# Optimization experiments

Measured on AMD Instinct MI355X. Metric: run time of the kernel, lower is better.

The kernel has to match this reference:

```python
import jax, jax.numpy as jnp
import numpy as np

N = 100000
E = 1600000
IN, HID, OUT = 128, 32, 32


def gcn_conv(x, ei, ew, W, b, n):
    # PyG GCNConv: symmetric norm with self-loops, edge_attr as edge weight
    h = x @ W                                  # [n, d_out]
    row, col = ei[0], ei[1]
    loop = jnp.arange(n)
    row = jnp.concatenate([row, loop])
    col = jnp.concatenate([col, loop])
    ew = jnp.concatenate([ew, jnp.ones((n,), ew.dtype)])
    deg = jax.ops.segment_sum(ew, col, num_segments=n)
    dinv = jnp.where(deg > 0, jax.lax.rsqrt(deg), 0.0)
    norm = dinv[row] * ew * dinv[col]          # [E+n]
    out = jax.ops.segment_sum(norm[:, None] * h[row], col, num_segments=n)
    return out + b


def setup_inputs() -> dict:
    key = jax.random.key(0)
    ks = jax.random.split(key, 24)
    inp = {}
    for i in range(3):
        inp[f"x{i+1}"] = jax.random.normal(ks[i], (N, IN), jnp.float32)
        inp[f"ei{i+1}"] = jax.random.randint(ks[3 + i], (2, E), 0, N, jnp.int64)
        inp[f"ea{i+1}"] = jax.random.uniform(ks[6 + i], (E,), jnp.float32)
        inp[f"W{i+1}"] = jax.random.normal(ks[9 + i], (IN, HID), jnp.float32) * (IN ** -0.5)
        inp[f"b{i+1}"] = jnp.zeros((HID,), jnp.float32)
        inp[f"Wo{i+1}"] = jax.random.normal(ks[12 + i], (HID, OUT), jnp.float32) * (HID ** -0.5)
        inp[f"bo{i+1}"] = jnp.zeros((OUT,), jnp.float32)
    inp["att_w"] = jax.random.normal(ks[15], (HID, 1), jnp.float32) * (HID ** -0.5)
    return inp


def reference(x1, x2, x3, ei1, ei2, ei3, ea1, ea2, ea3,
              W1, W2, W3, b1, b2, b3,
              Wo1, Wo2, Wo3, bo1, bo2, bo3, att_w):
    xs = [x1, x2, x3]
    eis = [ei1, ei2, ei3]
    eas = [ea1, ea2, ea3]
    Ws = [W1, W2, W3]
    bs = [b1, b2, b3]
    Wos = [Wo1, Wo2, Wo3]
    bos = [bo1, bo2, bo3]

    embs, coefs = [], []
    for x, ei, ea, W, b in zip(xs, eis, eas, Ws, bs):
        e = jax.nn.relu(gcn_conv(x, ei, ea, W, b, N))   # [N, HID]; dropout is eval no-op
        embs.append(e)
        coefs.append(jnp.exp(jax.nn.leaky_relu(e @ att_w)))  # [N, 1]
    coef_sum = coefs[0] + coefs[1] + coefs[2]
    weights = [c / coef_sum for c in coefs]
    h = sum(w * e for w, e in zip(weights, embs))       # [N, HID]

    out = sum(gcn_conv(h, ei, ea, Wo, bo, N)
              for ei, ea, Wo, bo in zip(eis, eas, Wos, bos))
    return (out, weights[0], weights[1], weights[2])
```

## Files before the change

### kernel.cpp

```cpp
#include <hip/hip_runtime.h>
#include <hip/hip_fp16.h>

typedef unsigned short u16;
typedef unsigned int   u32;
typedef _Float16 h2 __attribute__((ext_vector_type(2)));

#define N_NODES 100000
#define N_EDGES 1600000
#define IN_DIM  128
#define HID_DIM 32
#define OUT_DIM 32

#define BK   512
#define NBC  196
#define NBT  (3 * NBC)

#define PB    256
#define BINB  1024
#define CHUNK 18750
#define SC_N  (NBT * PB)
#define SC_CHUNK 2048
#define SC_G  ((SC_N + SC_CHUNK - 1) / SC_CHUNK)
#define GN4  ((N_NODES * 4 + 255) / 256)
#define MM2  ((N_NODES + 63) / 64)

#define KEYB 4
#define NKEY (BK << KEYB)

__device__ inline int ofs_at(const int* __restrict__ rp1, const int* __restrict__ bs, int m) {
    return m ? rp1[m] + bs[(m - 1) >> 11] : 0;
}


__global__ void binhist_kernel(const int* __restrict__ ei0, const int* __restrict__ ei1,
                               const int* __restrict__ ei2, int* __restrict__ hist_t) {
    __shared__ int hloc[NBT];
    for (int i = threadIdx.x; i < NBT; i += blockDim.x) hloc[i] = 0;
    __syncthreads();
    int b = blockIdx.x;
    int beg = b * CHUNK, end = beg + CHUNK;
    for (int e = beg + threadIdx.x; e < end; e += blockDim.x) {
        int c = (e >= 2 * N_EDGES) ? 2 : (e >= N_EDGES ? 1 : 0);
        const int* ei = (c == 0) ? ei0 : (c == 1) ? ei1 : ei2;
        int col = ei[N_EDGES + (e - c * N_EDGES)];
        atomicAdd(&hloc[c * NBC + (col >> 9)], 1);
    }
    __syncthreads();
    for (int g = threadIdx.x; g < NBT; g += blockDim.x)
        hist_t[g * PB + b] = hloc[g];
}


__global__ void scan1_kernel(const int* __restrict__ counts, int* __restrict__ rp1,
                             int* __restrict__ blocksum) {
    __shared__ int wsum[4];
    int tid = threadIdx.x;
    int base = blockIdx.x * SC_CHUNK + tid * 8;
    int vals[8];
    int tsum = 0;
    if (base < SC_N) {
        int4 v0 = *(const int4*)(counts + base);
        int4 v1 = *(const int4*)(counts + base + 4);
        vals[0] = v0.x; vals[1] = v0.y; vals[2] = v0.z; vals[3] = v0.w;
        vals[4] = v1.x; vals[5] = v1.y; vals[6] = v1.z; vals[7] = v1.w;
#pragma unroll
        for (int k = 0; k < 8; k++) tsum += vals[k];
    } else {
#pragma unroll
        for (int k = 0; k < 8; k++) vals[k] = 0;
    }
    int lane = tid & 63, wave = tid >> 6;
    int x = tsum;
    for (int d = 1; d < 64; d <<= 1) {
        int t = __shfl_up(x, d, 64);
        if (lane >= d) x += t;
    }
    if (lane == 63) wsum[wave] = x;
    __syncthreads();
    int woff = 0;
    for (int w = 0; w < wave; w++) woff += wsum[w];
    int run = woff + x - tsum;
    if (base < SC_N) {
#pragma unroll
        for (int k = 0; k < 8; k++) {
            run += vals[k];
            rp1[base + k + 1] = run;
        }
    }
    if (tid == blockDim.x - 1) blocksum[blockIdx.x] = woff + x;
    if (blockIdx.x == 0 && tid == 0) rp1[0] = 0;
}

__global__ void scan2_kernel(int* __restrict__ blocksum, int n) {
    __shared__ int wsum[4];
    int tid = threadIdx.x;
    int lane = tid & 63, wave = tid >> 6;
    int carry = 0;
    for (int base = 0; base < n; base += 256) {
        int i = base + tid;
        int v = (i < n) ? blocksum[i] : 0;
        int x = v;
        for (int d = 1; d < 64; d <<= 1) {
            int t = __shfl_up(x, d, 64);
            if (lane >= d) x += t;
        }
        if (lane == 63) wsum[wave] = x;
        __syncthreads();
        int woff = 0;
        for (int w = 0; w < wave; w++) woff += wsum[w];
        int total = wsum[0] + wsum[1] + wsum[2] + wsum[3];
        if (i < n) blocksum[i] = carry + woff + x - v;
        carry += total;
        __syncthreads();
    }
}


__global__ void binscatter_kernel(const int* __restrict__ ei0, const int* __restrict__ ei1,
                                  const int* __restrict__ ei2,
                                  const float* __restrict__ ea0, const float* __restrict__ ea1,
                                  const float* __restrict__ ea2,
                                  const int* __restrict__ rp1, const int* __restrict__ bsum,
                                  int2* __restrict__ stg) {
    __shared__ int base_l[NBT];
    int b = blockIdx.x;
    for (int g = threadIdx.x; g < NBT; g += blockDim.x)
        base_l[g] = ofs_at(rp1, bsum, g * PB + b);
    __syncthreads();
    int beg = b * CHUNK, end = beg + CHUNK;
    for (int e = beg + threadIdx.x; e < end; e += blockDim.x) {
        int c = (e >= 2 * N_EDGES) ? 2 : (e >= N_EDGES ? 1 : 0);
        int le = e - c * N_EDGES;
        const int* ei = (c == 0) ? ei0 : (c == 1) ? ei1 : ei2;
        const float* ea = (c == 0) ? ea0 : (c == 1) ? ea1 : ea2;
        int row = ei[le];
        int col = ei[N_EDGES + le];
        int g = c * NBC + (col >> 9);
        int slot = atomicAdd(&base_l[g], 1);
        stg[slot] = make_int2(row | ((col & 511) << 17), __float_as_int(ea[le]));
    }
}


__global__ void bucket_sort_kernel(const int2* __restrict__ stg, const int* __restrict__ rp1,
                                   const int* __restrict__ bsum,
                                   u32* __restrict__ csr,
                                   float* __restrict__ dinv, int* __restrict__ row_ptr) {
    __shared__ int hist[NKEY];
    __shared__ int colStart[BK];
    __shared__ float deg[BK];
    __shared__ float dl[BK];
    __shared__ int wsum[4];
    int tid = threadIdx.x;
    int g = blockIdx.x;
    int c = g / NBC;
    int colBase = (g % NBC) << 9;
    for (int i = tid; i < NKEY; i += 256) hist[i] = 0;
    deg[tid] = 1.0f;
    deg[tid + 256] = 1.0f;
    __syncthreads();
    int beg = ofs_at(rp1, bsum, g * PB);
    int end = (g == NBT - 1) ? 3 * N_EDGES : ofs_at(rp1, bsum, (g + 1) * PB);
    int cnt = end - beg;
    for (int i = tid; i < cnt; i += blockDim.x) {
        int2 p = stg[beg + i];
        int cl = (p.x >> 17) & 511;
        int row = p.x & 0x1FFFF;
        atomicAdd(&hist[(cl << KEYB) | (row >> 13)], 1);
        atomicAdd(&deg[cl], __int_as_float(p.y));
    }
    __syncthreads();
    int base32 = tid * 32;
    int v[32]; int tsum = 0;
#pragma unroll
    for (int k = 0; k < 32; k++) { v[k] = hist[base32 + k]; tsum += v[k]; }
    int lane = tid & 63, wave = tid >> 6;
    int xs = tsum;
    for (int d = 1; d < 64; d <<= 1) {
        int tt = __shfl_up(xs, d, 64);
        if (lane >= d) xs += tt;
    }
    if (lane == 63) wsum[wave] = xs;
    __syncthreads();
    int woff = 0;
    for (int w = 0; w < wave; w++) woff += wsum[w];
    int run = woff + xs - tsum;
#pragma unroll
    for (int k = 0; k < 32; k++) {
        if (k == 0)  colStart[2 * tid]     = run;
        if (k == 16) colStart[2 * tid + 1] = run;
        int t2 = v[k]; hist[base32 + k] = run; run += t2;
    }
    dl[tid] = rsqrtf(deg[tid]);
    dl[tid + 256] = rsqrtf(deg[tid + 256]);
    __syncthreads();
    for (int i = tid; i < cnt; i += blockDim.x) {
        int2 p = stg[beg + i];
        int cl = (p.x >> 17) & 511;
        int row = p.x & 0x1FFFF;
        int key = (cl << KEYB) | (row >> 13);
        int slot = atomicAdd(&hist[key], 1);
        float vv = __int_as_float(p.y) * dl[cl];
        __half h = __float2half(vv);
        u32 hb = (u32)(*(u16*)&h) & 0x7FFF;
        csr[beg + slot] = (u32)row | (hb << 17);
    }
#pragma unroll
    for (int q = 0; q < 2; q++) {
        int cl = tid + q * 256;
        int col = colBase + cl;
        if (col < N_NODES) {
            dinv[(size_t)c * N_NODES + col] = dl[cl];
            row_ptr[(size_t)c * N_NODES + col] = beg + colStart[cl];
        }
    }
    if (g == NBT - 1 && tid == 0) row_ptr[3 * N_NODES] = 3 * N_EDGES;
}


__device__ inline u32 pack_half2(float a, float b) {
    __half2 h = __floats2half2_rn(a, b);
    union { __half2 h; u32 u; } cv; cv.h = h;
    return cv.u;
}

__device__ inline float2 unpack_half2(u32 u) {
    union { u32 u; __half2 h; } cv; cv.u = u;
    return __half22float2(cv.h);
}

__device__ inline float val15(u32 meta) {
    return unpack_half2(meta >> 17).x;
}

__device__ inline float fdot2h(u32 a, u32 b, float c) {
    union { u32 u; h2 h; } ca, cb; ca.u = a; cb.u = b;
    return __builtin_amdgcn_fdot2(ca.h, cb.h, c, false);
}


__global__ void matmul_in3_kernel(const float* __restrict__ x0, const float* __restrict__ x1,
                                  const float* __restrict__ x2,
                                  const float* __restrict__ W0, const float* __restrict__ W1,
                                  const float* __restrict__ W2,
                                  const float* __restrict__ dinv,
                                  u16* __restrict__ h3) {
    __shared__ u32 Ws2[(IN_DIM / 2) * HID_DIM];
    int c = blockIdx.x / MM2;
    int lb = blockIdx.x % MM2;
    const float* x = (c == 0) ? x0 : (c == 1) ? x1 : x2;
    const float* W = (c == 0) ? W0 : (c == 1) ? W1 : W2;
    for (int i = threadIdx.x; i < (IN_DIM / 2) * HID_DIM; i += blockDim.x) {
        int d = i & 31, jp = i >> 5;
        Ws2[i] = pack_half2(W[(2 * jp) * HID_DIM + d], W[(2 * jp + 1) * HID_DIM + d]);
    }
    __syncthreads();
    int t = threadIdx.x & 7;
    int grp = threadIdx.x >> 3;
    int v0 = lb * 64 + grp * 2;
    if (v0 >= N_NODES) return;
    float a[2][4];
#pragma unroll
    for (int k = 0; k < 2; k++)
#pragma unroll
        for (int d = 0; d < 4; d++) a[k][d] = 0.f;
    const float* xr0 = x + (size_t)v0 * IN_DIM;
    const float* xr1 = xr0 + IN_DIM;
#pragma unroll 4
    for (int q = 0; q < 32; q++) {
        float4 xv0 = *(const float4*)(xr0 + 4 * q);
        float4 xv1 = *(const float4*)(xr1 + 4 * q);
        u32 p00 = pack_half2(xv0.x, xv0.y), p01 = pack_half2(xv0.z, xv0.w);
        u32 p10 = pack_half2(xv1.x, xv1.y), p11 = pack_half2(xv1.z, xv1.w);
        uint4 wA = *(const uint4*)&Ws2[(2 * q) * HID_DIM + 4 * t];
        uint4 wB = *(const uint4*)&Ws2[(2 * q + 1) * HID_DIM + 4 * t];
        a[0][0] = fdot2h(p00, wA.x, a[0][0]); a[0][1] = fdot2h(p00, wA.y, a[0][1]);
        a[0][2] = fdot2h(p00, wA.z, a[0][2]); a[0][3] = fdot2h(p00, wA.w, a[0][3]);
        a[0][0] = fdot2h(p01, wB.x, a[0][0]); a[0][1] = fdot2h(p01, wB.y, a[0][1]);
        a[0][2] = fdot2h(p01, wB.z, a[0][2]); a[0][3] = fdot2h(p01, wB.w, a[0][3]);
        a[1][0] = fdot2h(p10, wA.x, a[1][0]); a[1][1] = fdot2h(p10, wA.y, a[1][1]);
        a[1][2] = fdot2h(p10, wA.z, a[1][2]); a[1][3] = fdot2h(p10, wA.w, a[1][3]);
        a[1][0] = fdot2h(p11, wB.x, a[1][0]); a[1][1] = fdot2h(p11, wB.y, a[1][1]);
        a[1][2] = fdot2h(p11, wB.z, a[1][2]); a[1][3] = fdot2h(p11, wB.w, a[1][3]);
    }
#pragma unroll
    for (int k = 0; k < 2; k++) {
        float s = dinv[(size_t)c * N_NODES + v0 + k];
        uint2 pk = make_uint2(pack_half2(a[k][0] * s, a[k][1] * s),
                              pack_half2(a[k][2] * s, a[k][3] * s));
        *(uint2*)(h3 + ((size_t)c * N_NODES + v0 + k) * HID_DIM + 4 * t) = pk;
    }
}


__global__ void matmul_hid3_kernel(const float* __restrict__ hmix,
                                   const float* __restrict__ Wo0, const float* __restrict__ Wo1,
                                   const float* __restrict__ Wo2,
                                   const float* __restrict__ dinv,
                                   u16* __restrict__ h23) {
    __shared__ u32 Ws2[(HID_DIM / 2) * OUT_DIM];
    int c = blockIdx.x / MM2;
    int lb = blockIdx.x % MM2;
    const float* Wo = (c == 0) ? Wo0 : (c == 1) ? Wo1 : Wo2;
    for (int i = threadIdx.x; i < (HID_DIM / 2) * OUT_DIM; i += blockDim.x) {
        int d = i & 31, jp = i >> 5;
        Ws2[i] = pack_half2(Wo[(2 * jp) * OUT_DIM + d], Wo[(2 * jp + 1) * OUT_DIM + d]);
    }
    __syncthreads();
    int t = threadIdx.x & 7;
    int grp = threadIdx.x >> 3;
    int v0 = lb * 64 + grp * 2;
    if (v0 >= N_NODES) return;
    float a[2][4];
#pragma unroll
    for (int k = 0; k < 2; k++)
#pragma unroll
        for (int d = 0; d < 4; d++) a[k][d] = 0.f;
    const float* hr0 = hmix + (size_t)v0 * HID_DIM;
    const float* hr1 = hr0 + HID_DIM;
#pragma unroll
    for (int q = 0; q < 8; q++) {
        float4 xv0 = *(const float4*)(hr0 + 4 * q);
        float4 xv1 = *(const float4*)(hr1 + 4 * q);
        u32 p00 = pack_half2(xv0.x, xv0.y), p01 = pack_half2(xv0.z, xv0.w);
        u32 p10 = pack_half2(xv1.x, xv1.y), p11 = pack_half2(xv1.z, xv1.w);
        uint4 wA = *(const uint4*)&Ws2[(2 * q) * OUT_DIM + 4 * t];
        uint4 wB = *(const uint4*)&Ws2[(2 * q + 1) * OUT_DIM + 4 * t];
        a[0][0] = fdot2h(p00, wA.x, a[0][0]); a[0][1] = fdot2h(p00, wA.y, a[0][1]);
        a[0][2] = fdot2h(p00, wA.z, a[0][2]); a[0][3] = fdot2h(p00, wA.w, a[0][3]);
        a[0][0] = fdot2h(p01, wB.x, a[0][0]); a[0][1] = fdot2h(p01, wB.y, a[0][1]);
        a[0][2] = fdot2h(p01, wB.z, a[0][2]); a[0][3] = fdot2h(p01, wB.w, a[0][3]);
        a[1][0] = fdot2h(p10, wA.x, a[1][0]); a[1][1] = fdot2h(p10, wA.y, a[1][1]);
        a[1][2] = fdot2h(p10, wA.z, a[1][2]); a[1][3] = fdot2h(p10, wA.w, a[1][3]);
        a[1][0] = fdot2h(p11, wB.x, a[1][0]); a[1][1] = fdot2h(p11, wB.y, a[1][1]);
        a[1][2] = fdot2h(p11, wB.z, a[1][2]); a[1][3] = fdot2h(p11, wB.w, a[1][3]);
    }
#pragma unroll
    for (int k = 0; k < 2; k++) {
        float s = dinv[(size_t)c * N_NODES + v0 + k];
        uint2 pk = make_uint2(pack_half2(a[k][0] * s, a[k][1] * s),
                              pack_half2(a[k][2] * s, a[k][3] * s));
        *(uint2*)(h23 + ((size_t)c * N_NODES + v0 + k) * OUT_DIM + 4 * t) = pk;
    }
}


__global__ void gather_combine_kernel(const int* __restrict__ row_ptr,
                                      const u32* __restrict__ csr,
                                      const u16* __restrict__ h3,
                                      const float* __restrict__ dinv,
                                      const float* __restrict__ b0,
                                      const float* __restrict__ b1,
                                      const float* __restrict__ b2,
                                      const float* __restrict__ att_w,
                                      float* __restrict__ hmix,
                                      float* __restrict__ wout) {
    int gid = blockIdx.x * blockDim.x + threadIdx.x;
    int v = gid >> 2;
    int t = gid & 3;
    if (v >= N_NODES) return;
    float4 wv0 = *(const float4*)(att_w + t * 8);
    float4 wv1 = *(const float4*)(att_w + t * 8 + 4);
    float e[3][8];
    float coef[3];
#pragma unroll
    for (int c = 0; c < 3; c++) {
        const u16* h = h3 + (size_t)c * N_NODES * HID_DIM;
        const float* bb = (c == 0) ? b0 : (c == 1) ? b1 : b2;
        int beg = row_ptr[c * N_NODES + v], end = row_ptr[c * N_NODES + v + 1];
        float a[8];
#pragma unroll
        for (int k = 0; k < 8; k++) a[k] = 0.f;
        int ee = beg;
        for (; ee + 4 <= end; ee += 4) {
            u32 m0 = csr[ee], m1 = csr[ee + 1], m2 = csr[ee + 2], m3 = csr[ee + 3];
            uint4 u0 = *(const uint4*)(h + (size_t)(m0 & 0x1FFFF) * HID_DIM + 8 * t);
            uint4 u1 = *(const uint4*)(h + (size_t)(m1 & 0x1FFFF) * HID_DIM + 8 * t);
            uint4 u2 = *(const uint4*)(h + (size_t)(m2 & 0x1FFFF) * HID_DIM + 8 * t);
            uint4 u3 = *(const uint4*)(h + (size_t)(m3 & 0x1FFFF) * HID_DIM + 8 * t);
            float vl0 = val15(m0), vl1 = val15(m1), vl2 = val15(m2), vl3 = val15(m3);
            float2 f;
            f = unpack_half2(u0.x); a[0] += vl0 * f.x; a[1] += vl0 * f.y;
            f = unpack_half2(u0.y); a[2] += vl0 * f.x; a[3] += vl0 * f.y;
            f = unpack_half2(u0.z); a[4] += vl0 * f.x; a[5] += vl0 * f.y;
            f = unpack_half2(u0.w); a[6] += vl0 * f.x; a[7] += vl0 * f.y;
            f = unpack_half2(u1.x); a[0] += vl1 * f.x; a[1] += vl1 * f.y;
            f = unpack_half2(u1.y); a[2] += vl1 * f.x; a[3] += vl1 * f.y;
            f = unpack_half2(u1.z); a[4] += vl1 * f.x; a[5] += vl1 * f.y;
            f = unpack_half2(u1.w); a[6] += vl1 * f.x; a[7] += vl1 * f.y;
            f = unpack_half2(u2.x); a[0] += vl2 * f.x; a[1] += vl2 * f.y;
            f = unpack_half2(u2.y); a[2] += vl2 * f.x; a[3] += vl2 * f.y;
            f = unpack_half2(u2.z); a[4] += vl2 * f.x; a[5] += vl2 * f.y;
            f = unpack_half2(u2.w); a[6] += vl2 * f.x; a[7] += vl2 * f.y;
            f = unpack_half2(u3.x); a[0] += vl3 * f.x; a[1] += vl3 * f.y;
            f = unpack_half2(u3.y); a[2] += vl3 * f.x; a[3] += vl3 * f.y;
            f = unpack_half2(u3.z); a[4] += vl3 * f.x; a[5] += vl3 * f.y;
            f = unpack_half2(u3.w); a[6] += vl3 * f.x; a[7] += vl3 * f.y;
        }
        for (; ee < end; ee++) {
            u32 m = csr[ee];
            float vl = val15(m);
            uint4 u = *(const uint4*)(h + (size_t)(m & 0x1FFFF) * HID_DIM + 8 * t);
            float2 f;
            f = unpack_half2(u.x); a[0] += vl * f.x; a[1] += vl * f.y;
            f = unpack_half2(u.y); a[2] += vl * f.x; a[3] += vl * f.y;
            f = unpack_half2(u.z); a[4] += vl * f.x; a[5] += vl * f.y;
            f = unpack_half2(u.w); a[6] += vl * f.x; a[7] += vl * f.y;
        }
        float s = dinv[(size_t)c * N_NODES + v];
        uint4 u = *(const uint4*)(h + (size_t)v * HID_DIM + 8 * t);
        float2 f0 = unpack_half2(u.x), f1 = unpack_half2(u.y);
        float2 f2 = unpack_half2(u.z), f3 = unpack_half2(u.w);
        float4 bv0 = *(const float4*)(bb + t * 8);
        float4 bv1 = *(const float4*)(bb + t * 8 + 4);
        e[c][0] = fmaxf(a[0] + s * f0.x + bv0.x, 0.f);
        e[c][1] = fmaxf(a[1] + s * f0.y + bv0.y, 0.f);
        e[c][2] = fmaxf(a[2] + s * f1.x + bv0.z, 0.f);
        e[c][3] = fmaxf(a[3] + s * f1.y + bv0.w, 0.f);
        e[c][4] = fmaxf(a[4] + s * f2.x + bv1.x, 0.f);
        e[c][5] = fmaxf(a[5] + s * f2.y + bv1.y, 0.f);
        e[c][6] = fmaxf(a[6] + s * f3.x + bv1.z, 0.f);
        e[c][7] = fmaxf(a[7] + s * f3.y + bv1.w, 0.f);
        float dot = e[c][0] * wv0.x + e[c][1] * wv0.y + e[c][2] * wv0.z + e[c][3] * wv0.w
                  + e[c][4] * wv1.x + e[c][5] * wv1.y + e[c][6] * wv1.z + e[c][7] * wv1.w;
        dot += __shfl_xor(dot, 1, 64);
        dot += __shfl_xor(dot, 2, 64);
        float lr = (dot > 0.0f) ? dot : 0.01f * dot;
        coef[c] = expf(lr);
    }
    float inv = 1.0f / (coef[0] + coef[1] + coef[2]);
    float w0 = coef[0] * inv, w1 = coef[1] * inv, w2 = coef[2] * inv;
    if (t == 0) {
        wout[v] = w0;
        wout[N_NODES + v] = w1;
        wout[2 * N_NODES + v] = w2;
    }
    float4 r0, r1;
    r0.x = w0 * e[0][0] + w1 * e[1][0] + w2 * e[2][0];
    r0.y = w0 * e[0][1] + w1 * e[1][1] + w2 * e[2][1];
    r0.z = w0 * e[0][2] + w1 * e[1][2] + w2 * e[2][2];
    r0.w = w0 * e[0][3] + w1 * e[1][3] + w2 * e[2][3];
    r1.x = w0 * e[0][4] + w1 * e[1][4] + w2 * e[2][4];
    r1.y = w0 * e[0][5] + w1 * e[1][5] + w2 * e[2][5];
    r1.z = w0 * e[0][6] + w1 * e[1][6] + w2 * e[2][6];
    r1.w = w0 * e[0][7] + w1 * e[1][7] + w2 * e[2][7];
    *(float4*)(hmix + (size_t)v * HID_DIM + t * 8) = r0;
    *(float4*)(hmix + (size_t)v * HID_DIM + t * 8 + 4) = r1;
}


__global__ void gather_out_kernel(const int* __restrict__ row_ptr,
                                  const u32* __restrict__ csr,
                                  const u16* __restrict__ h23,
                                  const float* __restrict__ dinv,
                                  const float* __restrict__ bo0,
                                  const float* __restrict__ bo1,
                                  const float* __restrict__ bo2,
                                  float* __restrict__ out) {
    int gid = blockIdx.x * blockDim.x + threadIdx.x;
    int v = gid >> 2;
    int t = gid & 3;
    if (v >= N_NODES) return;
    float4 p0 = *(const float4*)(bo0 + t * 8);
    float4 p1 = *(const float4*)(bo0 + t * 8 + 4);
    float4 q0 = *(const float4*)(bo1 + t * 8);
    float4 q1 = *(const float4*)(bo1 + t * 8 + 4);
    float4 s0 = *(const float4*)(bo2 + t * 8);
    float4 s1 = *(const float4*)(bo2 + t * 8 + 4);
    float a[8];
    a[0] = p0.x + q0.x + s0.x; a[1] = p0.y + q0.y + s0.y;
    a[2] = p0.z + q0.z + s0.z; a[3] = p0.w + q0.w + s0.w;
    a[4] = p1.x + q1.x + s1.x; a[5] = p1.y + q1.y + s1.y;
    a[6] = p1.z + q1.z + s1.z; a[7] = p1.w + q1.w + s1.w;
#pragma unroll
    for (int c = 0; c < 3; c++) {
        const u16* h2m = h23 + (size_t)c * N_NODES * OUT_DIM;
        int beg = row_ptr[c * N_NODES + v], end = row_ptr[c * N_NODES + v + 1];
        int ee = beg;
        for (; ee + 4 <= end; ee += 4) {
            u32 m0 = csr[ee], m1 = csr[ee + 1], m2 = csr[ee + 2], m3 = csr[ee + 3];
            uint4 u0 = *(const uint4*)(h2m + (size_t)(m0 & 0x1FFFF) * OUT_DIM + 8 * t);
            uint4 u1 = *(const uint4*)(h2m + (size_t)(m1 & 0x1FFFF) * OUT_DIM + 8 * t);
            uint4 u2 = *(const uint4*)(h2m + (size_t)(m2 & 0x1FFFF) * OUT_DIM + 8 * t);
            uint4 u3 = *(const uint4*)(h2m + (size_t)(m3 & 0x1FFFF) * OUT_DIM + 8 * t);
            float vl0 = val15(m0), vl1 = val15(m1), vl2 = val15(m2), vl3 = val15(m3);
            float2 f;
            f = unpack_half2(u0.x); a[0] += vl0 * f.x; a[1] += vl0 * f.y;
            f = unpack_half2(u0.y); a[2] += vl0 * f.x; a[3] += vl0 * f.y;
            f = unpack_half2(u0.z); a[4] += vl0 * f.x; a[5] += vl0 * f.y;
            f = unpack_half2(u0.w); a[6] += vl0 * f.x; a[7] += vl0 * f.y;
            f = unpack_half2(u1.x); a[0] += vl1 * f.x; a[1] += vl1 * f.y;
            f = unpack_half2(u1.y); a[2] += vl1 * f.x; a[3] += vl1 * f.y;
            f = unpack_half2(u1.z); a[4] += vl1 * f.x; a[5] += vl1 * f.y;
            f = unpack_half2(u1.w); a[6] += vl1 * f.x; a[7] += vl1 * f.y;
            f = unpack_half2(u2.x); a[0] += vl2 * f.x; a[1] += vl2 * f.y;
            f = unpack_half2(u2.y); a[2] += vl2 * f.x; a[3] += vl2 * f.y;
            f = unpack_half2(u2.z); a[4] += vl2 * f.x; a[5] += vl2 * f.y;
            f = unpack_half2(u2.w); a[6] += vl2 * f.x; a[7] += vl2 * f.y;
            f = unpack_half2(u3.x); a[0] += vl3 * f.x; a[1] += vl3 * f.y;
            f = unpack_half2(u3.y); a[2] += vl3 * f.x; a[3] += vl3 * f.y;
            f = unpack_half2(u3.z); a[4] += vl3 * f.x; a[5] += vl3 * f.y;
            f = unpack_half2(u3.w); a[6] += vl3 * f.x; a[7] += vl3 * f.y;
        }
        for (; ee < end; ee++) {
            u32 m = csr[ee];
            float vl = val15(m);
            uint4 u = *(const uint4*)(h2m + (size_t)(m & 0x1FFFF) * OUT_DIM + 8 * t);
            float2 f;
            f = unpack_half2(u.x); a[0] += vl * f.x; a[1] += vl * f.y;
            f = unpack_half2(u.y); a[2] += vl * f.x; a[3] += vl * f.y;
            f = unpack_half2(u.z); a[4] += vl * f.x; a[5] += vl * f.y;
            f = unpack_half2(u.w); a[6] += vl * f.x; a[7] += vl * f.y;
        }
        float s = dinv[(size_t)c * N_NODES + v];
        uint4 u = *(const uint4*)(h2m + (size_t)v * OUT_DIM + 8 * t);
        float2 f0 = unpack_half2(u.x), f1 = unpack_half2(u.y);
        float2 f2 = unpack_half2(u.z), f3 = unpack_half2(u.w);
        a[0] += s * f0.x; a[1] += s * f0.y; a[2] += s * f1.x; a[3] += s * f1.y;
        a[4] += s * f2.x; a[5] += s * f2.y; a[6] += s * f3.x; a[7] += s * f3.y;
    }
    float4 o0, o1;
    o0.x = a[0]; o0.y = a[1]; o0.z = a[2]; o0.w = a[3];
    o1.x = a[4]; o1.y = a[5]; o1.z = a[6]; o1.w = a[7];
    *(float4*)(out + (size_t)v * OUT_DIM + t * 8) = o0;
    *(float4*)(out + (size_t)v * OUT_DIM + t * 8 + 4) = o1;
}


extern "C" void kernel_launch(void* const* d_in, const int* in_sizes, int n_in,
                              void* d_out, int out_size, void* d_ws, size_t ws_size,
                              hipStream_t stream) {
    const float* x[3];  const int* ei[3];  const float* ea[3];
    const float* W[3];  const float* b[3]; const float* Wo[3]; const float* bo[3];
    for (int c = 0; c < 3; c++) {
        x[c]  = (const float*)d_in[7 * c + 0];
        ei[c] = (const int*)  d_in[7 * c + 1];
        ea[c] = (const float*)d_in[7 * c + 2];
        W[c]  = (const float*)d_in[7 * c + 3];
        b[c]  = (const float*)d_in[7 * c + 4];
        Wo[c] = (const float*)d_in[7 * c + 5];
        bo[c] = (const float*)d_in[7 * c + 6];
    }
    const float* att_w = (const float*)d_in[21];
    float* out = (float*)d_out;
    float* wout = out + (size_t)N_NODES * OUT_DIM;

    int*   wsb      = (int*)d_ws;
    float* dinv     = (float*)wsb;
    int*   row_ptr  = wsb + 3 * N_NODES;
    int*   blocksum = row_ptr + 3 * N_NODES + 4;
    size_t stg_off  = (size_t)(3 * N_NODES + 3 * N_NODES + 4 + 512);
    stg_off = (stg_off + 3) & ~(size_t)3;
    int2*  stg      = (int2*)(wsb + stg_off);
    u32*   csr      = (u32*)(stg + 3 * (size_t)N_EDGES);
    u16*   hA       = (u16*)(csr + 3 * (size_t)N_EDGES);
    int*   hist_t   = (int*)hA;
    int*   rp1      = hist_t + SC_N;
    float* hmix     = (float*)(hA + 3 * (size_t)N_NODES * HID_DIM);

    const int B = 256;

    binhist_kernel<<<PB, BINB, 0, stream>>>(ei[0], ei[1], ei[2], hist_t);
    scan1_kernel<<<SC_G, B, 0, stream>>>(hist_t, rp1, blocksum);
    scan2_kernel<<<1, B, 0, stream>>>(blocksum, SC_G);
    binscatter_kernel<<<PB, BINB, 0, stream>>>(ei[0], ei[1], ei[2], ea[0], ea[1], ea[2],
                                               rp1, blocksum, stg);
    bucket_sort_kernel<<<NBT, B, 0, stream>>>(stg, rp1, blocksum, csr, dinv, row_ptr);

    matmul_in3_kernel<<<3 * MM2, B, 0, stream>>>(x[0], x[1], x[2], W[0], W[1], W[2],
                                                 dinv, hA);
    gather_combine_kernel<<<GN4, B, 0, stream>>>(row_ptr, csr, hA, dinv,
                                                 b[0], b[1], b[2], att_w, hmix, wout);

    matmul_hid3_kernel<<<3 * MM2, B, 0, stream>>>(hmix, Wo[0], Wo[1], Wo[2], dinv, hA);
    gather_out_kernel<<<GN4, B, 0, stream>>>(row_ptr, csr, hA, dinv,
                                             bo[0], bo[1], bo[2], out);
}
```

Before: 562.5 us.

## Split fused per-graph gathers into one launch per graph for cache locality

The fused gather kernels, which walked all three graphs per node, are split into separate per-graph launches. Graph embeddings go through an fp16 buffer placed in the staging area, and a separate combine kernel applies the attention weights. The output gather accumulates into the output buffer across launches. The aim is a smaller feature working set per launch (one graph's h at a time) so the random gathers hit L2/MALL more often. The cost is extra launches, extra intermediate traffic, and one more fp16 rounding of the embeddings.

```diff
diff --git a/kernel.cpp b/kernel.cpp
--- a/kernel.cpp
+++ b/kernel.cpp
@@ -345,16 +345,82 @@
 }
 
 
-__global__ void gather_combine_kernel(const int* __restrict__ row_ptr,
-                                      const u32* __restrict__ csr,
-                                      const u16* __restrict__ h3,
-                                      const float* __restrict__ dinv,
-                                      const float* __restrict__ b0,
-                                      const float* __restrict__ b1,
-                                      const float* __restrict__ b2,
-                                      const float* __restrict__ att_w,
-                                      float* __restrict__ hmix,
-                                      float* __restrict__ wout) {
+__global__ void gather_e_kernel(const int* __restrict__ row_ptr,
+                                const u32* __restrict__ csr,
+                                const u16* __restrict__ h3,
+                                const float* __restrict__ dinv,
+                                const float* __restrict__ bb,
+                                u16* __restrict__ ebuf, int c) {
+    int gid = blockIdx.x * blockDim.x + threadIdx.x;
+    int v = gid >> 2;
+    int t = gid & 3;
+    if (v >= N_NODES) return;
+    const u16* h = h3 + (size_t)c * N_NODES * HID_DIM;
+    int beg = row_ptr[c * N_NODES + v], end = row_ptr[c * N_NODES + v + 1];
+    float a[8];
+#pragma unroll
+    for (int k = 0; k < 8; k++) a[k] = 0.f;
+    int ee = beg;
+    for (; ee + 4 <= end; ee += 4) {
+        u32 m0 = csr[ee], m1 = csr[ee + 1], m2 = csr[ee + 2], m3 = csr[ee + 3];
+        uint4 u0 = *(const uint4*)(h + (size_t)(m0 & 0x1FFFF) * HID_DIM + 8 * t);
+        uint4 u1 = *(const uint4*)(h + (size_t)(m1 & 0x1FFFF) * HID_DIM + 8 * t);
+        uint4 u2 = *(const uint4*)(h + (size_t)(m2 & 0x1FFFF) * HID_DIM + 8 * t);
+        uint4 u3 = *(const uint4*)(h + (size_t)(m3 & 0x1FFFF) * HID_DIM + 8 * t);
+        float vl0 = val15(m0), vl1 = val15(m1), vl2 = val15(m2), vl3 = val15(m3);
+        float2 f;
+        f = unpack_half2(u0.x); a[0] += vl0 * f.x; a[1] += vl0 * f.y;
+        f = unpack_half2(u0.y); a[2] += vl0 * f.x; a[3] += vl0 * f.y;
+        f = unpack_half2(u0.z); a[4] += vl0 * f.x; a[5] += vl0 * f.y;
+        f = unpack_half2(u0.w); a[6] += vl0 * f.x; a[7] += vl0 * f.y;
+        f = unpack_half2(u1.x); a[0] += vl1 * f.x; a[1] += vl1 * f.y;
+        f = unpack_half2(u1.y); a[2] += vl1 * f.x; a[3] += vl1 * f.y;
+        f = unpack_half2(u1.z); a[4] += vl1 * f.x; a[5] += vl1 * f.y;
+        f = unpack_half2(u1.w); a[6] += vl1 * f.x; a[7] += vl1 * f.y;
+        f = unpack_half2(u2.x); a[0] += vl2 * f.x; a[1] += vl2 * f.y;
+        f = unpack_half2(u2.y); a[2] += vl2 * f.x; a[3] += vl2 * f.y;
+        f = unpack_half2(u2.z); a[4] += vl2 * f.x; a[5] += vl2 * f.y;
+        f = unpack_half2(u2.w); a[6] += vl2 * f.x; a[7] += vl2 * f.y;
+        f = unpack_half2(u3.x); a[0] += vl3 * f.x; a[1] += vl3 * f.y;
+        f = unpack_half2(u3.y); a[2] += vl3 * f.x; a[3] += vl3 * f.y;
+        f = unpack_half2(u3.z); a[4] += vl3 * f.x; a[5] += vl3 * f.y;
+        f = unpack_half2(u3.w); a[6] += vl3 * f.x; a[7] += vl3 * f.y;
+    }
+    for (; ee < end; ee++) {
+        u32 m = csr[ee];
+        float vl = val15(m);
+        uint4 u = *(const uint4*)(h + (size_t)(m & 0x1FFFF) * HID_DIM + 8 * t);
+        float2 f;
+        f = unpack_half2(u.x); a[0] += vl * f.x; a[1] += vl * f.y;
+        f = unpack_half2(u.y); a[2] += vl * f.x; a[3] += vl * f.y;
+        f = unpack_half2(u.z); a[4] += vl * f.x; a[5] += vl * f.y;
+        f = unpack_half2(u.w); a[6] += vl * f.x; a[7] += vl * f.y;
+    }
+    float s = dinv[(size_t)c * N_NODES + v];
+    uint4 u = *(const uint4*)(h + (size_t)v * HID_DIM + 8 * t);
+    float2 f0 = unpack_half2(u.x), f1 = unpack_half2(u.y);
+    float2 f2 = unpack_half2(u.z), f3 = unpack_half2(u.w);
+    float4 bv0 = *(const float4*)(bb + t * 8);
+    float4 bv1 = *(const float4*)(bb + t * 8 + 4);
+    float e0 = fmaxf(a[0] + s * f0.x + bv0.x, 0.f);
+    float e1 = fmaxf(a[1] + s * f0.y + bv0.y, 0.f);
+    float e2 = fmaxf(a[2] + s * f1.x + bv0.z, 0.f);
+    float e3 = fmaxf(a[3] + s * f1.y + bv0.w, 0.f);
+    float e4 = fmaxf(a[4] + s * f2.x + bv1.x, 0.f);
+    float e5 = fmaxf(a[5] + s * f2.y + bv1.y, 0.f);
+    float e6 = fmaxf(a[6] + s * f3.x + bv1.z, 0.f);
+    float e7 = fmaxf(a[7] + s * f3.y + bv1.w, 0.f);
+    uint4 pk;
+    pk.x = pack_half2(e0, e1); pk.y = pack_half2(e2, e3);
+    pk.z = pack_half2(e4, e5); pk.w = pack_half2(e6, e7);
+    *(uint4*)(ebuf + ((size_t)c * N_NODES + v) * HID_DIM + 8 * t) = pk;
+}
+
+
+__global__ void combine_kernel(const u16* __restrict__ ebuf,
+                               const float* __restrict__ att_w,
+                               float* __restrict__ hmix,
+                               float* __restrict__ wout) {
     int gid = blockIdx.x * blockDim.x + threadIdx.x;
     int v = gid >> 2;
     int t = gid & 3;
@@ -365,62 +431,11 @@
     float coef[3];
 #pragma unroll
     for (int c = 0; c < 3; c++) {
-        const u16* h = h3 + (size_t)c * N_NODES * HID_DIM;
-        const float* bb = (c == 0) ? b0 : (c == 1) ? b1 : b2;
-        int beg = row_ptr[c * N_NODES + v], end = row_ptr[c * N_NODES + v + 1];
-        float a[8];
-#pragma unroll
-        for (int k = 0; k < 8; k++) a[k] = 0.f;
-        int ee = beg;
-        for (; ee + 4 <= end; ee += 4) {
-            u32 m0 = csr[ee], m1 = csr[ee + 1], m2 = csr[ee + 2], m3 = csr[ee + 3];
-            uint4 u0 = *(const uint4*)(h + (size_t)(m0 & 0x1FFFF) * HID_DIM + 8 * t);
-            uint4 u1 = *(const uint4*)(h + (size_t)(m1 & 0x1FFFF) * HID_DIM + 8 * t);
-            uint4 u2 = *(const uint4*)(h + (size_t)(m2 & 0x1FFFF) * HID_DIM + 8 * t);
-            uint4 u3 = *(const uint4*)(h + (size_t)(m3 & 0x1FFFF) * HID_DIM + 8 * t);
-            float vl0 = val15(m0), vl1 = val15(m1), vl2 = val15(m2), vl3 = val15(m3);
-            float2 f;
-            f = unpack_half2(u0.x); a[0] += vl0 * f.x; a[1] += vl0 * f.y;
-            f = unpack_half2(u0.y); a[2] += vl0 * f.x; a[3] += vl0 * f.y;
-            f = unpack_half2(u0.z); a[4] += vl0 * f.x; a[5] += vl0 * f.y;
-            f = unpack_half2(u0.w); a[6] += vl0 * f.x; a[7] += vl0 * f.y;
-            f = unpack_half2(u1.x); a[0] += vl1 * f.x; a[1] += vl1 * f.y;
-            f = unpack_half2(u1.y); a[2] += vl1 * f.x; a[3] += vl1 * f.y;
-            f = unpack_half2(u1.z); a[4] += vl1 * f.x; a[5] += vl1 * f.y;
-            f = unpack_half2(u1.w); a[6] += vl1 * f.x; a[7] += vl1 * f.y;
-            f = unpack_half2(u2.x); a[0] += vl2 * f.x; a[1] += vl2 * f.y;
-            f = unpack_half2(u2.y); a[2] += vl2 * f.x; a[3] += vl2 * f.y;
-            f = unpack_half2(u2.z); a[4] += vl2 * f.x; a[5] += vl2 * f.y;
-            f = unpack_half2(u2.w); a[6] += vl2 * f.x; a[7] += vl2 * f.y;
-            f = unpack_half2(u3.x); a[0] += vl3 * f.x; a[1] += vl3 * f.y;
-            f = unpack_half2(u3.y); a[2] += vl3 * f.x; a[3] += vl3 * f.y;
-            f = unpack_half2(u3.z); a[4] += vl3 * f.x; a[5] += vl3 * f.y;
-            f = unpack_half2(u3.w); a[6] += vl3 * f.x; a[7] += vl3 * f.y;
-        }
-        for (; ee < end; ee++) {
-            u32 m = csr[ee];
-            float vl = val15(m);
-            uint4 u = *(const uint4*)(h + (size_t)(m & 0x1FFFF) * HID_DIM + 8 * t);
-            float2 f;
-            f = unpack_half2(u.x); a[0] += vl * f.x; a[1] += vl * f.y;
-            f = unpack_half2(u.y); a[2] += vl * f.x; a[3] += vl * f.y;
-            f = unpack_half2(u.z); a[4] += vl * f.x; a[5] += vl * f.y;
-            f = unpack_half2(u.w); a[6] += vl * f.x; a[7] += vl * f.y;
-        }
-        float s = dinv[(size_t)c * N_NODES + v];
-        uint4 u = *(const uint4*)(h + (size_t)v * HID_DIM + 8 * t);
+        uint4 u = *(const uint4*)(ebuf + ((size_t)c * N_NODES + v) * HID_DIM + 8 * t);
         float2 f0 = unpack_half2(u.x), f1 = unpack_half2(u.y);
         float2 f2 = unpack_half2(u.z), f3 = unpack_half2(u.w);
-        float4 bv0 = *(const float4*)(bb + t * 8);
-        float4 bv1 = *(const float4*)(bb + t * 8 + 4);
-        e[c][0] = fmaxf(a[0] + s * f0.x + bv0.x, 0.f);
-        e[c][1] = fmaxf(a[1] + s * f0.y + bv0.y, 0.f);
-        e[c][2] = fmaxf(a[2] + s * f1.x + bv0.z, 0.f);
-        e[c][3] = fmaxf(a[3] + s * f1.y + bv0.w, 0.f);
-        e[c][4] = fmaxf(a[4] + s * f2.x + bv1.x, 0.f);
-        e[c][5] = fmaxf(a[5] + s * f2.y + bv1.y, 0.f);
-        e[c][6] = fmaxf(a[6] + s * f3.x + bv1.z, 0.f);
-        e[c][7] = fmaxf(a[7] + s * f3.y + bv1.w, 0.f);
+        e[c][0] = f0.x; e[c][1] = f0.y; e[c][2] = f1.x; e[c][3] = f1.y;
+        e[c][4] = f2.x; e[c][5] = f2.y; e[c][6] = f3.x; e[c][7] = f3.y;
         float dot = e[c][0] * wv0.x + e[c][1] * wv0.y + e[c][2] * wv0.z + e[c][3] * wv0.w
                   + e[c][4] * wv1.x + e[c][5] * wv1.y + e[c][6] * wv1.z + e[c][7] * wv1.w;
         dot += __shfl_xor(dot, 1, 64);
@@ -449,81 +464,93 @@
 }
 
 
-__global__ void gather_out_kernel(const int* __restrict__ row_ptr,
-                                  const u32* __restrict__ csr,
-                                  const u16* __restrict__ h23,
-                                  const float* __restrict__ dinv,
-                                  const float* __restrict__ bo0,
-                                  const float* __restrict__ bo1,
-                                  const float* __restrict__ bo2,
-                                  float* __restrict__ out) {
+__global__ void gather_out_c_kernel(const int* __restrict__ row_ptr,
+                                    const u32* __restrict__ csr,
+                                    const u16* __restrict__ h23,
+                                    const float* __restrict__ dinv,
+                                    const float* __restrict__ bo0,
+                                    const float* __restrict__ bo1,
+                                    const float* __restrict__ bo2,
+                                    float* __restrict__ out, int c) {
     int gid = blockIdx.x * blockDim.x + threadIdx.x;
     int v = gid >> 2;
     int t = gid & 3;
     if (v >= N_NODES) return;
-    float4 p0 = *(const float4*)(bo0 + t * 8);
-    float4 p1 = *(const float4*)(bo0 + t * 8 + 4);
-    float4 q0 = *(const float4*)(bo1 + t * 8);
-    float4 q1 = *(const float4*)(bo1 + t * 8 + 4);
-    float4 s0 = *(const float4*)(bo2 + t * 8);
-    float4 s1 = *(const float4*)(bo2 + t * 8 + 4);
     float a[8];
-    a[0] = p0.x + q0.x + s0.x; a[1] = p0.y + q0.y + s0.y;
-    a[2] = p0.z + q0.z + s0.z; a[3] = p0.w + q0.w + s0.w;
-    a[4] = p1.x + q1.x + s1.x; a[5] = p1.y + q1.y + s1.y;
-    a[6] = p1.z + q1.z + s1.z; a[7] = p1.w + q1.w + s1.w;
-#pragma unroll
-    for (int c = 0; c < 3; c++) {
-        const u16* h2m = h23 + (size_t)c * N_NODES * OUT_DIM;
-        int beg = row_ptr[c * N_NODES + v], end = row_ptr[c * N_NODES + v + 1];
-        int ee = beg;
-        for (; ee + 4 <= end; ee += 4) {
-            u32 m0 = csr[ee], m1 = csr[ee + 1], m2 = csr[ee + 2], m3 = csr[ee + 3];
-            uint4 u0 = *(const uint4*)(h2m + (size_t)(m0 & 0x1FFFF) * OUT_DIM + 8 * t);
-            uint4 u1 = *(const uint4*)(h2m + (size_t)(m1 & 0x1FFFF) * OUT_DIM + 8 * t);
-            uint4 u2 = *(const uint4*)(h2m + (size_t)(m2 & 0x1FFFF) * OUT_DIM + 8 * t);
-            uint4 u3 = *(const uint4*)(h2m + (size_t)(m3 & 0x1FFFF) * OUT_DIM + 8 * t);
-            float vl0 = val15(m0), vl1 = val15(m1), vl2 = val15(m2), vl3 = val15(m3);
-            float2 f;
-            f = unpack_half2(u0.x); a[0] += vl0 * f.x; a[1] += vl0 * f.y;
-            f = unpack_half2(u0.y); a[2] += vl0 * f.x; a[3] += vl0 * f.y;
-            f = unpack_half2(u0.z); a[4] += vl0 * f.x; a[5] += vl0 * f.y;
-            f = unpack_half2(u0.w); a[6] += vl0 * f.x; a[7] += vl0 * f.y;
-            f = unpack_half2(u1.x); a[0] += vl1 * f.x; a[1] += vl1 * f.y;
-            f = unpack_half2(u1.y); a[2] += vl1 * f.x; a[3] += vl1 * f.y;
-            f = unpack_half2(u1.z); a[4] += vl1 * f.x; a[5] += vl1 * f.y;
-            f = unpack_half2(u1.w); a[6] += vl1 * f.x; a[7] += vl1 * f.y;
-            f = unpack_half2(u2.x); a[0] += vl2 * f.x; a[1] += vl2 * f.y;
-            f = unpack_half2(u2.y); a[2] += vl2 * f.x; a[3] += vl2 * f.y;
-            f = unpack_half2(u2.z); a[4] += vl2 * f.x; a[5] += vl2 * f.y;
-            f = unpack_half2(u2.w); a[6] += vl2 * f.x; a[7] += vl2 * f.y;
-            f = unpack_half2(u3.x); a[0] += vl3 * f.x; a[1] += vl3 * f.y;
-            f = unpack_half2(u3.y); a[2] += vl3 * f.x; a[3] += vl3 * f.y;
-            f = unpack_half2(u3.z); a[4] += vl3 * f.x; a[5] += vl3 * f.y;
-            f = unpack_half2(u3.w); a[6] += vl3 * f.x; a[7] += vl3 * f.y;
-        }
-        for (; ee < end; ee++) {
-            u32 m = csr[ee];
-            float vl = val15(m);
-            uint4 u = *(const uint4*)(h2m + (size_t)(m & 0x1FFFF) * OUT_DIM + 8 * t);
-            float2 f;
-            f = unpack_half2(u.x); a[0] += vl * f.x; a[1] += vl * f.y;
-            f = unpack_half2(u.y); a[2] += vl * f.x; a[3] += vl * f.y;
-            f = unpack_half2(u.z); a[4] += vl * f.x; a[5] += vl * f.y;
-            f = unpack_half2(u.w); a[6] += vl * f.x; a[7] += vl * f.y;
-        }
-        float s = dinv[(size_t)c * N_NODES + v];
-        uint4 u = *(const uint4*)(h2m + (size_t)v * OUT_DIM + 8 * t);
-        float2 f0 = unpack_half2(u.x), f1 = unpack_half2(u.y);
-        float2 f2 = unpack_half2(u.z), f3 = unpack_half2(u.w);
-        a[0] += s * f0.x; a[1] += s * f0.y; a[2] += s * f1.x; a[3] += s * f1.y;
-        a[4] += s * f2.x; a[5] += s * f2.y; a[6] += s * f3.x; a[7] += s * f3.y;
-    }
-    float4 o0, o1;
-    o0.x = a[0]; o0.y = a[1]; o0.z = a[2]; o0.w = a[3];
-    o1.x = a[4]; o1.y = a[5]; o1.z = a[6]; o1.w = a[7];
-    *(float4*)(out + (size_t)v * OUT_DIM + t * 8) = o0;
-    *(float4*)(out + (size_t)v * OUT_DIM + t * 8 + 4) = o1;
+    if (c == 0) {
+        float4 p0 = *(const float4*)(bo0 + t * 8);
+        float4 p1 = *(const float4*)(bo0 + t * 8 + 4);
+        float4 q0 = *(const float4*)(bo1 + t * 8);
+        float4 q1 = *(const float4*)(bo1 + t * 8 + 4);
+        float4 s0 = *(const float4*)(bo2 + t * 8);
+        float4 s1 = *(const float4*)(bo2 + t * 8 + 4);
+        a[0] = p0.x + q0.x + s0.x; a[1] = p0.y + q0.y + s0.y;
+        a[2] = p0.z + q0.z + s0.z; a[3] = p0.w + q0.w + s0.w;
+        a[4] = p1.x + q1.x + s1.x; a[5] = p1.y + q1.y + s1.y;
+        a[6] = p1.z + q1.z + s1.z; a[7] = p1.w + q1.w + s1.w;
+    } else {
+#pragma unroll
+        for (int k = 0; k < 8; k++) a[k] = 0.f;
+    }
+    const u16* h2m = h23 + (size_t)c * N_NODES * OUT_DIM;
+    int beg = row_ptr[c * N_NODES + v], end = row_ptr[c * N_NODES + v + 1];
+    int ee = beg;
+    for (; ee + 4 <= end; ee += 4) {
+        u32 m0 = csr[ee], m1 = csr[ee + 1], m2 = csr[ee + 2], m3 = csr[ee + 3];
+        uint4 u0 = *(const uint4*)(h2m + (size_t)(m0 & 0x1FFFF) * OUT_DIM + 8 * t);
+        uint4 u1 = *(const uint4*)(h2m + (size_t)(m1 & 0x1FFFF) * OUT_DIM + 8 * t);
+        uint4 u2 = *(const uint4*)(h2m + (size_t)(m2 & 0x1FFFF) * OUT_DIM + 8 * t);
+        uint4 u3 = *(const uint4*)(h2m + (size_t)(m3 & 0x1FFFF) * OUT_DIM + 8 * t);
+        float vl0 = val15(m0), vl1 = val15(m1), vl2 = val15(m2), vl3 = val15(m3);
+        float2 f;
+        f = unpack_half2(u0.x); a[0] += vl0 * f.x; a[1] += vl0 * f.y;
+        f = unpack_half2(u0.y); a[2] += vl0 * f.x; a[3] += vl0 * f.y;
+        f = unpack_half2(u0.z); a[4] += vl0 * f.x; a[5] += vl0 * f.y;
+        f = unpack_half2(u0.w); a[6] += vl0 * f.x; a[7] += vl0 * f.y;
+        f = unpack_half2(u1.x); a[0] += vl1 * f.x; a[1] += vl1 * f.y;
+        f = unpack_half2(u1.y); a[2] += vl1 * f.x; a[3] += vl1 * f.y;
+        f = unpack_half2(u1.z); a[4] += vl1 * f.x; a[5] += vl1 * f.y;
+        f = unpack_half2(u1.w); a[6] += vl1 * f.x; a[7] += vl1 * f.y;
+        f = unpack_half2(u2.x); a[0] += vl2 * f.x; a[1] += vl2 * f.y;
+        f = unpack_half2(u2.y); a[2] += vl2 * f.x; a[3] += vl2 * f.y;
+        f = unpack_half2(u2.z); a[4] += vl2 * f.x; a[5] += vl2 * f.y;
+        f = unpack_half2(u2.w); a[6] += vl2 * f.x; a[7] += vl2 * f.y;
+        f = unpack_half2(u3.x); a[0] += vl3 * f.x; a[1] += vl3 * f.y;
+        f = unpack_half2(u3.y); a[2] += vl3 * f.x; a[3] += vl3 * f.y;
+        f = unpack_half2(u3.z); a[4] += vl3 * f.x; a[5] += vl3 * f.y;
+        f = unpack_half2(u3.w); a[6] += vl3 * f.x; a[7] += vl3 * f.y;
+    }
+    for (; ee < end; ee++) {
+        u32 m = csr[ee];
+        float vl = val15(m);
+        uint4 u = *(const uint4*)(h2m + (size_t)(m & 0x1FFFF) * OUT_DIM + 8 * t);
+        float2 f;
+        f = unpack_half2(u.x); a[0] += vl * f.x; a[1] += vl * f.y;
+        f = unpack_half2(u.y); a[2] += vl * f.x; a[3] += vl * f.y;
+        f = unpack_half2(u.z); a[4] += vl * f.x; a[5] += vl * f.y;
+        f = unpack_half2(u.w); a[6] += vl * f.x; a[7] += vl * f.y;
+    }
+    float s = dinv[(size_t)c * N_NODES + v];
+    uint4 u = *(const uint4*)(h2m + (size_t)v * OUT_DIM + 8 * t);
+    float2 f0 = unpack_half2(u.x), f1 = unpack_half2(u.y);
+    float2 f2 = unpack_half2(u.z), f3 = unpack_half2(u.w);
+    a[0] += s * f0.x; a[1] += s * f0.y; a[2] += s * f1.x; a[3] += s * f1.y;
+    a[4] += s * f2.x; a[5] += s * f2.y; a[6] += s * f3.x; a[7] += s * f3.y;
+    float* op = out + (size_t)v * OUT_DIM + t * 8;
+    if (c == 0) {
+        float4 o0, o1;
+        o0.x = a[0]; o0.y = a[1]; o0.z = a[2]; o0.w = a[3];
+        o1.x = a[4]; o1.y = a[5]; o1.z = a[6]; o1.w = a[7];
+        *(float4*)(op) = o0;
+        *(float4*)(op + 4) = o1;
+    } else {
+        float4 c0 = *(const float4*)(op);
+        float4 c1 = *(const float4*)(op + 4);
+        c0.x += a[0]; c0.y += a[1]; c0.z += a[2]; c0.w += a[3];
+        c1.x += a[4]; c1.y += a[5]; c1.z += a[6]; c1.w += a[7];
+        *(float4*)(op) = c0;
+        *(float4*)(op + 4) = c1;
+    }
 }
 
 
@@ -557,6 +584,7 @@
     int*   hist_t   = (int*)hA;
     int*   rp1      = hist_t + SC_N;
     float* hmix     = (float*)(hA + 3 * (size_t)N_NODES * HID_DIM);
+    u16*   ebuf     = (u16*)stg;
 
     const int B = 256;
 
@@ -569,10 +597,12 @@
 
     matmul_in3_kernel<<<3 * MM2, B, 0, stream>>>(x[0], x[1], x[2], W[0], W[1], W[2],
                                                  dinv, hA);
-    gather_combine_kernel<<<GN4, B, 0, stream>>>(row_ptr, csr, hA, dinv,
-                                                 b[0], b[1], b[2], att_w, hmix, wout);
+    for (int c = 0; c < 3; c++)
+        gather_e_kernel<<<GN4, B, 0, stream>>>(row_ptr, csr, hA, dinv, b[c], ebuf, c);
+    combine_kernel<<<GN4, B, 0, stream>>>(ebuf, att_w, hmix, wout);
 
     matmul_hid3_kernel<<<3 * MM2, B, 0, stream>>>(hmix, Wo[0], Wo[1], Wo[2], dinv, hA);
-    gather_out_kernel<<<GN4, B, 0, stream>>>(row_ptr, csr, hA, dinv,
-                                             bo[0], bo[1], bo[2], out);
-}
+    for (int c = 0; c < 3; c++)
+        gather_out_c_kernel<<<GN4, B, 0, stream>>>(row_ptr, csr, hA, dinv,
+                                                   bo[0], bo[1], bo[2], out, c);
+}
```

New measurement: 560.4 us. No clear change (-0.4%).
